# Performance work log

Measured on AMD Instinct MI355X. Metric: run time of the kernel, lower is better.

Reference implementation:

```python
import jax, jax.numpy as jnp
import numpy as np

NUM_PERS = 16
D = 128
N = 4096
EPSILON = 0.1
EPS_NORM = 1e-12  # matches torch F.normalize default eps


def setup_inputs() -> dict:
    key = jax.random.key(0)
    k1, k2 = jax.random.split(key)
    context = jax.random.normal(k1, (N, D), dtype=jnp.float32)
    # xavier_uniform for shape (num_pers, input_size): bound = sqrt(6/(fan_in+fan_out))
    bound = float(np.sqrt(6.0 / (NUM_PERS + D)))
    weight_tensor = jax.random.uniform(k2, (NUM_PERS, D), dtype=jnp.float32,
                                       minval=-bound, maxval=bound)
    return {"context": context, "weight_tensor": weight_tensor}


def reference(context, weight_tensor):
    # context: [N, D]; weight_tensor: [P, D]
    # per-perspective weighted features: [P, N, D]
    context_fc = context[None, :, :] * weight_tensor[:, None, :]
    # L2 normalize along feature dim (torch F.normalize: x / max(||x||, eps))
    norm = jnp.maximum(jnp.linalg.norm(context_fc, axis=-1, keepdims=True), EPS_NORM)
    context_norm = context_fc / norm
    # cosine similarity per perspective, mean over perspectives: [N, N]
    attention = jnp.einsum('pnd,pmd->pnm', context_norm, context_norm).mean(0)
    # epsilon neighbourhood with markoff_value = 0
    mask = (attention > EPSILON).astype(attention.dtype)
    return attention * mask
```

## Files before the change

### kernel.cpp

```cpp
#include <hip/hip_runtime.h>
#include <math.h>

#define N 4096
#define D 128
#define P 16
#define KK 2048
#define NT 32
#define NBLK (NT * (NT + 1) / 2)
#define LCAP 3072
#define CAP (1u << 20)
#define WIN 1.5e-3f
#define ZSCALE 256.0f
#define OSCALE (1.0f / 16777216.0f * 16.0f)

typedef _Float16 half_t;
typedef __attribute__((ext_vector_type(8))) _Float16 f16x8;
typedef __attribute__((ext_vector_type(4))) float f32x4;
typedef __attribute__((address_space(1))) const unsigned int* gptr_t;
typedef __attribute__((address_space(3))) unsigned int* lptr_t;

__global__ __launch_bounds__(256) void k_pack(const float* __restrict__ c,
                                              const float* __restrict__ w,
                                              double* __restrict__ rnorm,
                                              half_t* __restrict__ zb,
                                              unsigned* gcnt, unsigned* govf,
                                              int do_init) {
    int n = blockIdx.x, tid = threadIdx.x;
    if (do_init && n == 0 && tid == 0) { *gcnt = 0; *govf = 0; }
    int p = tid >> 4, d0 = (tid & 15) * 8;
    const float* cc = c + (size_t)n * D + d0;
    const float* ww = w + (size_t)p * D + d0;
    float cv[8], wv[8];
    *(float4*)&cv[0] = *(const float4*)&cc[0];
    *(float4*)&cv[4] = *(const float4*)&cc[4];
    *(float4*)&wv[0] = *(const float4*)&ww[0];
    *(float4*)&wv[4] = *(const float4*)&ww[4];
    double s = 0.0;
#pragma unroll
    for (int i = 0; i < 8; ++i) {
        double v = (double)cv[i] * (double)wv[i];
        s += v * v;
    }
#pragma unroll
    for (int o = 1; o < 16; o <<= 1) s += __shfl_xor(s, o, 64);
    double rn = 1.0 / fmax(sqrt(s), 1e-12);
    if ((tid & 15) == 0) rnorm[p * N + n] = rn;
    float rnf = (float)rn;
    f16x8 o8;
#pragma unroll
    for (int i = 0; i < 8; ++i) o8[i] = (half_t)(cv[i] * wv[i] * rnf * ZSCALE);
    *(f16x8*)&zb[(size_t)n * KK + tid * 8] = o8;
}

template <bool FUSED>
__global__ __launch_bounds__(256, 4) void k_gemm(const half_t* __restrict__ zb,
                                                 float* __restrict__ out,
                                                 unsigned* __restrict__ gcnt,
                                                 unsigned* __restrict__ govf,
                                                 unsigned* __restrict__ glist) {
    __shared__ __align__(16) half_t As[128 * 32];
    __shared__ __align__(16) half_t Bs[128 * 32];
    __shared__ unsigned lds_list[LCAP];
    __shared__ unsigned lds_cnt, lds_base, lds_tot;

    int tid = threadIdx.x;
    if (FUSED && tid == 0) lds_cnt = 0;

    int lane = tid & 63, wv = tid >> 6;
    int wr = wv >> 1, wc = wv & 1;

    int braw = blockIdx.x;
    int b = (braw & 7) * (NBLK / 8) + (braw >> 3);
    int ti = 0;
    while (b >= NT - ti) { b -= NT - ti; ++ti; }
    int tj = ti + b;
    int n0 = ti * 128, m0 = tj * 128;

    f32x4 acc[4][4] = {};
    int lrow = lane >> 2;
    int lchunk = (((lane & 3) ^ (lrow & 3)) * 8);

    for (int k0 = 0; k0 < KK; k0 += 32) {
#pragma unroll
        for (int h = 0; h < 2; ++h) {
            int s = h * 4 + wv;
            int row = s * 16 + lrow;
            __builtin_amdgcn_global_load_lds((gptr_t)(zb + (size_t)(n0 + row) * KK + k0 + lchunk),
                                             (lptr_t)(As + s * 512), 16, 0, 0);
            __builtin_amdgcn_global_load_lds((gptr_t)(zb + (size_t)(m0 + row) * KK + k0 + lchunk),
                                             (lptr_t)(Bs + s * 512), 16, 0, 0);
        }
        __syncthreads();

        f16x8 af[4], bfr[4];
        int kk_c = lane >> 4;
        int rsel = lane & 15;
        int kphys = (kk_c ^ (rsel & 3)) * 8;
#pragma unroll
        for (int f = 0; f < 4; ++f) {
            af[f]  = *(f16x8*)&As[(wr * 64 + f * 16 + rsel) * 32 + kphys];
            bfr[f] = *(f16x8*)&Bs[(wc * 64 + f * 16 + rsel) * 32 + kphys];
        }
#pragma unroll
        for (int i = 0; i < 4; ++i)
#pragma unroll
            for (int j = 0; j < 4; ++j)
                acc[i][j] = __builtin_amdgcn_mfma_f32_16x16x32_f16(af[i], bfr[j], acc[i][j], 0, 0, 0);
        __syncthreads();
    }

    int colD = lane & 15, rq = lane >> 4;
    bool mir = (ti != tj);
#pragma unroll
    for (int i = 0; i < 4; ++i)
#pragma unroll
        for (int j = 0; j < 4; ++j) {
            int rbase = n0 + wr * 64 + i * 16 + rq * 4;
            int ccol = m0 + wc * 64 + j * 16 + colD;
            float4 mv;
#pragma unroll
            for (int q = 0; q < 4; ++q) {
                float a = acc[i][j][q] * OSCALE;
                float sv;
                if (FUSED) {
                    bool flg = fabsf(a - 0.1f) < WIN;
                    sv = flg ? a : (a > 0.1f ? a : 0.0f);
                    if (flg) {
                        unsigned pos = atomicAdd(&lds_cnt, 1u);
                        unsigned ent = (unsigned)(rbase + q) | ((unsigned)ccol << 12) |
                                       (mir ? (1u << 24) : 0u);
                        if (pos < LCAP) lds_list[pos] = ent;
                    }
                } else {
                    sv = a;
                }
                out[(size_t)(rbase + q) * N + ccol] = sv;
                ((float*)&mv)[q] = sv;
            }
            if (mir) *(float4*)&out[(size_t)ccol * N + rbase] = mv;
        }

    if (FUSED) {
        __syncthreads();
        if (tid == 0) {
            unsigned tot = lds_cnt;
            unsigned cnt = tot > LCAP ? LCAP : tot;
            lds_tot = cnt;
            lds_base = atomicAdd(gcnt, cnt);
            if (tot > LCAP) atomicOr(govf, 1u);
        }
        __syncthreads();
        unsigned cnt = lds_tot, base = lds_base;
        for (unsigned e = tid; e < cnt; e += 256) {
            unsigned gi = base + e;
            if (gi < CAP) glist[gi] = lds_list[e];
            else atomicOr(govf, 1u);
        }
    }
}

__global__ __launch_bounds__(256) void k_fix2(const float* __restrict__ c,
                                              const float* __restrict__ w,
                                              const double* __restrict__ rnorm,
                                              const unsigned* __restrict__ gcnt,
                                              const unsigned* __restrict__ glist,
                                              float* __restrict__ out) {
    __shared__ double w2[D * P];
    for (int e = threadIdx.x; e < P * D; e += 256) {
        int p = e >> 7, d = e & 127;
        double wv = (double)w[p * D + d];
        w2[d * P + p] = wv * wv;
    }
    __syncthreads();

    unsigned count = *gcnt;
    if (count > CAP) count = CAP;
    unsigned stride = gridDim.x * 256;
    for (unsigned e = blockIdx.x * 256 + threadIdx.x; e < count; e += stride) {
        unsigned u = glist[e];
        int n = u & 4095, m = (u >> 12) & 4095;
        const float* cn = c + (size_t)n * D;
        const float* cm = c + (size_t)m * D;
        double acc[P];
#pragma unroll
        for (int p = 0; p < P; ++p) acc[p] = 0.0;
        for (int d0 = 0; d0 < D; d0 += 4) {
            float4 a4 = *(const float4*)&cn[d0];
            float4 b4 = *(const float4*)&cm[d0];
            float av[4] = {a4.x, a4.y, a4.z, a4.w};
            float bv[4] = {b4.x, b4.y, b4.z, b4.w};
#pragma unroll
            for (int q = 0; q < 4; ++q) {
                double pr = (double)av[q] * (double)bv[q];
#pragma unroll
                for (int p = 0; p < P; ++p) acc[p] += pr * w2[(d0 + q) * P + p];
            }
        }
        double t = 0.0;
#pragma unroll
        for (int p = 0; p < P; ++p)
            t += acc[p] * (rnorm[p * N + n] * rnorm[p * N + m]);
        double fin = t * 0.0625;
        float res = (fin > 0.1) ? (float)fin : 0.0f;
        out[(size_t)n * N + m] = res;
        if (u >> 24) out[(size_t)m * N + n] = res;
    }
}

__global__ __launch_bounds__(256) void k_guard(const float* __restrict__ c,
                                               const float* __restrict__ w,
                                               const double* __restrict__ rnorm,
                                               const unsigned* __restrict__ govf,
                                               float* __restrict__ out) {
    if (*govf == 0) return;
    __shared__ double w2[D * P];
    for (int e = threadIdx.x; e < P * D; e += 256) {
        int p = e >> 7, d = e & 127;
        double wv = (double)w[p * D + d];
        w2[d * P + p] = wv * wv;
    }
    __syncthreads();
    size_t stride = (size_t)gridDim.x * 256;
    for (size_t idx = (size_t)blockIdx.x * 256 + threadIdx.x; idx < (size_t)N * N;
         idx += stride) {
        float a = out[idx];
        if (fabsf(a - 0.1f) >= WIN) {
            out[idx] = (a > 0.1f) ? a : 0.0f;
            continue;
        }
        int n = (int)(idx >> 12), m = (int)(idx & (N - 1));
        const float* cn = c + (size_t)n * D;
        const float* cm = c + (size_t)m * D;
        double acc[P];
#pragma unroll
        for (int p = 0; p < P; ++p) acc[p] = 0.0;
        for (int d0 = 0; d0 < D; d0 += 4) {
            float4 a4 = *(const float4*)&cn[d0];
            float4 b4 = *(const float4*)&cm[d0];
            float av[4] = {a4.x, a4.y, a4.z, a4.w};
            float bv[4] = {b4.x, b4.y, b4.z, b4.w};
#pragma unroll
            for (int q = 0; q < 4; ++q) {
                double pr = (double)av[q] * (double)bv[q];
#pragma unroll
                for (int p = 0; p < P; ++p) acc[p] += pr * w2[(d0 + q) * P + p];
            }
        }
        double t = 0.0;
#pragma unroll
        for (int p = 0; p < P; ++p)
            t += acc[p] * (rnorm[p * N + n] * rnorm[p * N + m]);
        double fin = t * 0.0625;
        out[idx] = (fin > 0.1) ? (float)fin : 0.0f;
    }
}

__global__ __launch_bounds__(256) void k_fix_full(const float* __restrict__ c,
                                                  const float* __restrict__ w,
                                                  const double* __restrict__ rnorm,
                                                  float* __restrict__ out) {
    __shared__ double w2[D * P];
    for (int e = threadIdx.x; e < P * D; e += 256) {
        int p = e >> 7, d = e & 127;
        double wv = (double)w[p * D + d];
        w2[d * P + p] = wv * wv;
    }
    __syncthreads();
    size_t stride = (size_t)gridDim.x * 256;
    for (size_t idx = (size_t)blockIdx.x * 256 + threadIdx.x; idx < (size_t)N * N;
         idx += stride) {
        float a = out[idx];
        if (fabsf(a - 0.1f) >= WIN) {
            out[idx] = (a > 0.1f) ? a : 0.0f;
            continue;
        }
        int n = (int)(idx >> 12), m = (int)(idx & (N - 1));
        const float* cn = c + (size_t)n * D;
        const float* cm = c + (size_t)m * D;
        double acc[P];
#pragma unroll
        for (int p = 0; p < P; ++p) acc[p] = 0.0;
        for (int d0 = 0; d0 < D; d0 += 4) {
            float4 a4 = *(const float4*)&cn[d0];
            float4 b4 = *(const float4*)&cm[d0];
            float av[4] = {a4.x, a4.y, a4.z, a4.w};
            float bv[4] = {b4.x, b4.y, b4.z, b4.w};
#pragma unroll
            for (int q = 0; q < 4; ++q) {
                double pr = (double)av[q] * (double)bv[q];
#pragma unroll
                for (int p = 0; p < P; ++p) acc[p] += pr * w2[(d0 + q) * P + p];
            }
        }
        double t = 0.0;
#pragma unroll
        for (int p = 0; p < P; ++p)
            t += acc[p] * (rnorm[p * N + n] * rnorm[p * N + m]);
        double fin = t * 0.0625;
        out[idx] = (fin > 0.1) ? (float)fin : 0.0f;
    }
}

extern "C" void kernel_launch(void* const* d_in, const int* in_sizes, int n_in,
                              void* d_out, int out_size, void* d_ws, size_t ws_size,
                              hipStream_t stream) {
    const float* c = (const float*)d_in[0];
    const float* w = (const float*)d_in[1];
    float* out = (float*)d_out;
    char* ws = (char*)d_ws;

    double* rnorm = (double*)ws;
    size_t off = (size_t)P * N * 8;
    unsigned* gcnt = (unsigned*)(ws + off);
    unsigned* govf = gcnt + 1;
    unsigned* glist = (unsigned*)(ws + off + 128);
    half_t* zb = (half_t*)(ws + off + 128 + (size_t)CAP * 4);
    size_t need = off + 128 + (size_t)CAP * 4 + (size_t)N * KK * 2;

    if (ws_size >= need) {
        k_pack<<<N, 256, 0, stream>>>(c, w, rnorm, zb, gcnt, govf, 1);
        k_gemm<true><<<NBLK, 256, 0, stream>>>(zb, out, gcnt, govf, glist);
        k_fix2<<<1024, 256, 0, stream>>>(c, w, rnorm, gcnt, glist, out);
        k_guard<<<1024, 256, 0, stream>>>(c, w, rnorm, govf, out);
    } else {
        half_t* zb2 = (half_t*)(ws + off);
        k_pack<<<N, 256, 0, stream>>>(c, w, rnorm, zb2, nullptr, nullptr, 0);
        k_gemm<false><<<NBLK, 256, 0, stream>>>(zb2, out, nullptr, nullptr, nullptr);
        k_fix_full<<<4096, 256, 0, stream>>>(c, w, rnorm, out);
    }
}
```

Measured before the change: 100.3 us.

## Double-buffer LDS tiles in GEMM and re-swizzle LDS layout

The GEMM main loop now keeps two LDS buffers for A and B. The global-to-LDS loads for the next K-slice are issued before the MFMAs on the current slice, so each iteration has one barrier instead of two. The XOR swizzle now uses row>>1, which suits the 64-byte row pitch and is meant to cut LDS bank conflicts. The per-block candidate list capacity is cut from 3072 to 2048 so the extra LDS still fits at four blocks per CU. That raises the risk of list overflow and more use of the global fallback path.

```diff
diff --git a/kernel.cpp b/kernel.cpp
--- a/kernel.cpp
+++ b/kernel.cpp
@@ -7,7 +7,7 @@
 #define KK 2048
 #define NT 32
 #define NBLK (NT * (NT + 1) / 2)
-#define LCAP 3072
+#define LCAP 2048
 #define CAP (1u << 20)
 #define WIN 1.5e-3f
 #define ZSCALE 256.0f
@@ -58,8 +58,8 @@
                                                  unsigned* __restrict__ gcnt,
                                                  unsigned* __restrict__ govf,
                                                  unsigned* __restrict__ glist) {
-    __shared__ __align__(16) half_t As[128 * 32];
-    __shared__ __align__(16) half_t Bs[128 * 32];
+    __shared__ __align__(16) half_t As[2][128 * 32];
+    __shared__ __align__(16) half_t Bs[2][128 * 32];
     __shared__ unsigned lds_list[LCAP];
     __shared__ unsigned lds_cnt, lds_base, lds_tot;
 
@@ -78,34 +78,46 @@
 
     f32x4 acc[4][4] = {};
     int lrow = lane >> 2;
-    int lchunk = (((lane & 3) ^ (lrow & 3)) * 8);
-
-    for (int k0 = 0; k0 < KK; k0 += 32) {
+    int lchunk = (((lane & 3) ^ ((lrow >> 1) & 3)) * 8);
+
+    auto STAGE = [&](int buf, int k0) {
 #pragma unroll
         for (int h = 0; h < 2; ++h) {
             int s = h * 4 + wv;
             int row = s * 16 + lrow;
-            __builtin_amdgcn_global_load_lds((gptr_t)(zb + (size_t)(n0 + row) * KK + k0 + lchunk),
-                                             (lptr_t)(As + s * 512), 16, 0, 0);
-            __builtin_amdgcn_global_load_lds((gptr_t)(zb + (size_t)(m0 + row) * KK + k0 + lchunk),
-                                             (lptr_t)(Bs + s * 512), 16, 0, 0);
-        }
-        __syncthreads();
+            __builtin_amdgcn_global_load_lds(
+                (gptr_t)(zb + (size_t)(n0 + row) * KK + k0 + lchunk),
+                (lptr_t)(&As[buf][s * 512]), 16, 0, 0);
+            __builtin_amdgcn_global_load_lds(
+                (gptr_t)(zb + (size_t)(m0 + row) * KK + k0 + lchunk),
+                (lptr_t)(&Bs[buf][s * 512]), 16, 0, 0);
+        }
+    };
+
+    int kk_c = lane >> 4;
+    int rsel = lane & 15;
+    int kphys = (kk_c ^ ((rsel >> 1) & 3)) * 8;
+
+    STAGE(0, 0);
+    __syncthreads();
+
+#pragma unroll 2
+    for (int t = 0; t < 64; ++t) {
+        int cur = t & 1;
+        if (t < 63) STAGE(cur ^ 1, (t + 1) * 32);
 
         f16x8 af[4], bfr[4];
-        int kk_c = lane >> 4;
-        int rsel = lane & 15;
-        int kphys = (kk_c ^ (rsel & 3)) * 8;
 #pragma unroll
         for (int f = 0; f < 4; ++f) {
-            af[f]  = *(f16x8*)&As[(wr * 64 + f * 16 + rsel) * 32 + kphys];
-            bfr[f] = *(f16x8*)&Bs[(wc * 64 + f * 16 + rsel) * 32 + kphys];
+            af[f]  = *(f16x8*)&As[cur][(wr * 64 + f * 16 + rsel) * 32 + kphys];
+            bfr[f] = *(f16x8*)&Bs[cur][(wc * 64 + f * 16 + rsel) * 32 + kphys];
         }
 #pragma unroll
         for (int i = 0; i < 4; ++i)
 #pragma unroll
             for (int j = 0; j < 4; ++j)
                 acc[i][j] = __builtin_amdgcn_mfma_f32_16x16x32_f16(af[i], bfr[j], acc[i][j], 0, 0, 0);
+
         __syncthreads();
     }
 
```

Measured after the change: 105.9 us. +5.5%, slower.
